# Optimization experiments

Hardware: AMD Instinct MI355X
Metric: run time of the kernel (lower is better)

## Reference

```python
import jax, jax.numpy as jnp
import numpy as np

Z_SIZE, X_SIZE = 12, 32
B, NUM_HEADS, DIM = 16, 8, 256
N = Z_SIZE * Z_SIZE + X_SIZE * X_SIZE  # 1168


def _gen_rel_index(z, x):
    # 2D concatenated (template+search) relative position index, as in the torch helper
    zh, zw = np.meshgrid(np.arange(z), np.arange(z), indexing='ij')
    xh, xw = np.meshgrid(np.arange(x), np.arange(x), indexing='ij')
    h = np.concatenate([zh.ravel(), xh.ravel()])
    w = np.concatenate([zw.ravel(), xw.ravel()])
    dh = h[:, None] - h[None, :]
    dw = w[:, None] - w[None, :]
    a = np.concatenate([np.zeros(z * z, np.int64), np.ones(x * x, np.int64)])
    n = a.shape[0]
    b = np.broadcast_to(a[:, None], (n, n))
    c = np.broadcast_to(a[None, :], (n, n))
    diff = np.stack([dh, dw, b, c], axis=-1).reshape(-1, 4)
    _, inv = np.unique(diff, axis=0, return_inverse=True)
    return inv.reshape(n, n).astype(np.int32)


def setup_inputs() -> dict:
    key = jax.random.key(0)
    k0, k1, k2, k3, k4, k5 = jax.random.split(key, 6)
    x = jax.random.normal(k0, (B, N, DIM), jnp.float32)
    mask = jax.random.randint(k1, (B, N), 0, 2) > 0  # True = masked-out key
    w_qkv = jax.random.normal(k2, (3 * DIM, DIM), jnp.float32) * 0.02
    w_proj = jax.random.normal(k3, (DIM, DIM), jnp.float32) * 0.02
    b_proj = jax.random.normal(k4, (DIM,), jnp.float32) * 0.02
    rel_index = jnp.asarray(_gen_rel_index(Z_SIZE, X_SIZE))
    num_rel = int(rel_index.max()) + 1
    rpb_table = jax.random.normal(k5, (NUM_HEADS, num_rel), jnp.float32) * 0.02
    return {"x": x, "mask": mask, "w_qkv": w_qkv, "w_proj": w_proj,
            "b_proj": b_proj, "rpb_table": rpb_table, "rel_index": rel_index}


def reference(x, mask, w_qkv, w_proj, b_proj, rpb_table, rel_index):
    Bb, Nn, C = x.shape
    H = rpb_table.shape[0]
    Dh = C // H
    scale = Dh ** -0.5
    qkv = (x @ w_qkv.T).reshape(Bb, Nn, 3, H, Dh)
    qkv = jnp.transpose(qkv, (2, 0, 3, 1, 4))  # [3, B, H, N, Dh]
    q, k, v = qkv[0], qkv[1], qkv[2]
    attn = jnp.einsum('bhnd,bhmd->bhnm', q, k) * scale
    attn = attn + rpb_table[:, rel_index][None]           # gathered rel-pos bias [1,H,N,N]
    attn = jnp.where(mask[:, None, None, :], -jnp.inf, attn)
    attn = jax.nn.softmax(attn, axis=-1)
    out = jnp.einsum('bhnm,bhmd->bnhd', attn, v).reshape(Bb, Nn, C)
    return out @ w_proj.T + b_proj
```

## Files before the change

kernel.cpp:

```cpp
#include <hip/hip_runtime.h>
#include <hip/hip_bf16.h>

#define BATCH 16
#define NH 8
#define NSEQ 1168
#define NPAD 1184
#define DH 32
#define DMODEL 256
#define MTOK (BATCH*NSEQ)
#define LOG2E 1.4426950408889634f
#define QSCALE_L2 (0.17677669529663687f * 1.4426950408889634f)
#define NRELCAP 8448

typedef __bf16 bf16_t;
typedef __bf16 bf16x8 __attribute__((ext_vector_type(8)));
typedef __bf16 bf16x4 __attribute__((ext_vector_type(4)));
typedef __bf16 bf16x2 __attribute__((ext_vector_type(2)));
typedef float  f32x4  __attribute__((ext_vector_type(4)));

__device__ __forceinline__ f32x4 mfma16(bf16x8 a, bf16x8 b, f32x4 c) {
    return __builtin_amdgcn_mfma_f32_16x16x32_bf16(a, b, c, 0, 0, 0);
}

__device__ __forceinline__ float fexp2(float x) {
#if __has_builtin(__builtin_amdgcn_exp2f)
    return __builtin_amdgcn_exp2f(x);
#else
    return exp2f(x);
#endif
}

__global__ __launch_bounds__(256) void mask_probe(const unsigned char* __restrict__ m,
                                                  int* __restrict__ flag) {
    int nbytes = BATCH * NSEQ;
    int stride = gridDim.x * blockDim.x;
    int acc = 0;
    for (int i = blockIdx.x * blockDim.x + threadIdx.x; i < nbytes; i += stride)
        if ((i & 3) && m[i]) acc = 1;
    if (__any(acc)) {
        if ((threadIdx.x & 63) == 0) atomicOr(flag, 1);
    }
}

__global__ __launch_bounds__(256) void mask_expand(const void* __restrict__ mraw,
                                                   const int* __restrict__ flag,
                                                   unsigned short* __restrict__ mask16) {
    int t = blockIdx.x * blockDim.x + threadIdx.x;
    if (t >= BATCH * NPAD) return;
    int b = t / NPAD, k = t - b * NPAD;
    bool masked = true;
    if (k < NSEQ) {
        if (*flag) masked = ((const unsigned char*)mraw)[b * NSEQ + k] != 0;
        else       masked = ((const int*)mraw)[b * NSEQ + k] != 0;
    }
    mask16[t] = masked ? 0u : 0xFFFFu;
}

__global__ __launch_bounds__(256) void bias_build(
    const int* __restrict__ rel, const float* __restrict__ rpb,
    bf16_t* __restrict__ bias, int num_rel) {
    __shared__ float rpb_s[NRELCAP];
    int h = blockIdx.y;
    const float* rph = rpb + (size_t)h * num_rel;
    int nr = num_rel > NRELCAP ? NRELCAP : num_rel;
    for (int i = threadIdx.x; i < nr; i += 256) rpb_s[i] = rph[i] * LOG2E;
    __syncthreads();
    int q0 = blockIdx.x * 32;
    int qend = q0 + 32 > NSEQ ? NSEQ : q0 + 32;
    for (int q = q0; q < qend; ++q) {
        bf16_t* brow = bias + ((size_t)h * NSEQ + q) * NPAD;
        const int* rrow = rel + (size_t)q * NSEQ;
        for (int k4 = threadIdx.x * 4; k4 < NPAD; k4 += 1024) {
            bf16x4 w;
            if (k4 + 3 < NSEQ) {
                int4 r4 = *(const int4*)&rrow[k4];
                w[0] = (bf16_t)rpb_s[r4.x]; w[1] = (bf16_t)rpb_s[r4.y];
                w[2] = (bf16_t)rpb_s[r4.z]; w[3] = (bf16_t)rpb_s[r4.w];
            } else {
                #pragma unroll
                for (int j = 0; j < 4; ++j) {
                    int k = k4 + j;
                    w[j] = (bf16_t)((k < NSEQ) ? rpb_s[rrow[k]] : -1e30f);
                }
            }
            *(bf16x4*)&brow[k4] = w;
        }
    }
}

__global__ __launch_bounds__(256) void convert_kernel(
    const float* __restrict__ x, const float* __restrict__ wq, const float* __restrict__ wp,
    bf16_t* __restrict__ xb, bf16_t* __restrict__ wqb, bf16_t* __restrict__ wpb) {
    const int NX4 = MTOK*DMODEL/4, NQ4 = 768*256/4, NP4 = 256*256/4;
    int stride = gridDim.x * blockDim.x;
    int tid = blockIdx.x * blockDim.x + threadIdx.x;
    for (int i = tid; i < NX4; i += stride) {
        float4 f = ((const float4*)x)[i];
        bf16x4 o = { (bf16_t)f.x, (bf16_t)f.y, (bf16_t)f.z, (bf16_t)f.w };
        ((bf16x4*)xb)[i] = o;
    }
    for (int i = tid; i < NQ4; i += stride) {
        float4 f = ((const float4*)wq)[i];
        bf16x4 o = { (bf16_t)f.x, (bf16_t)f.y, (bf16_t)f.z, (bf16_t)f.w };
        ((bf16x4*)wqb)[i] = o;
    }
    for (int i = tid; i < NP4; i += stride) {
        float4 f = ((const float4*)wp)[i];
        bf16x4 o = { (bf16_t)f.x, (bf16_t)f.y, (bf16_t)f.z, (bf16_t)f.w };
        ((bf16x4*)wpb)[i] = o;
    }
}

#define GEMM_CORE(Aptr, Bptr) \
    __shared__ bf16_t As[128*32]; \
    __shared__ bf16_t Bs[128*32]; \
    int t = threadIdx.x; \
    int rowA0 = blockIdx.x * 128, rowB0 = blockIdx.y * 128; \
    int lane = t & 63, w = t >> 6; \
    int wr = (w >> 1) * 64, wc = (w & 1) * 64; \
    int lr = lane & 15, lg = lane >> 4; \
    int srow = t >> 2, scol = (t & 3) * 8; \
    f32x4 acc[4][4]; \
    { f32x4 zz = {0.f,0.f,0.f,0.f}; \
      _Pragma("unroll") for (int m = 0; m < 4; ++m) \
      _Pragma("unroll") for (int n = 0; n < 4; ++n) acc[m][n] = zz; } \
    for (int k0 = 0; k0 < 256; k0 += 32) { \
        bf16x8 ra0 = *(const bf16x8*)&Aptr[(size_t)(rowA0 + srow) * 256 + k0 + scol]; \
        bf16x8 ra1 = *(const bf16x8*)&Aptr[(size_t)(rowA0 + 64 + srow) * 256 + k0 + scol]; \
        bf16x8 rb0 = *(const bf16x8*)&Bptr[(size_t)(rowB0 + srow) * 256 + k0 + scol]; \
        bf16x8 rb1 = *(const bf16x8*)&Bptr[(size_t)(rowB0 + 64 + srow) * 256 + k0 + scol]; \
        __syncthreads(); \
        *(bf16x8*)&As[srow * 32 + scol] = ra0; \
        *(bf16x8*)&As[(64 + srow) * 32 + scol] = ra1; \
        *(bf16x8*)&Bs[srow * 32 + scol] = rb0; \
        *(bf16x8*)&Bs[(64 + srow) * 32 + scol] = rb1; \
        __syncthreads(); \
        bf16x8 af[4], bfr[4]; \
        _Pragma("unroll") for (int m = 0; m < 4; ++m) \
            af[m] = *(const bf16x8*)&As[(wr + m * 16 + lr) * 32 + lg * 8]; \
        _Pragma("unroll") for (int n = 0; n < 4; ++n) \
            bfr[n] = *(const bf16x8*)&Bs[(wc + n * 16 + lr) * 32 + lg * 8]; \
        _Pragma("unroll") for (int m = 0; m < 4; ++m) \
        _Pragma("unroll") for (int n = 0; n < 4; ++n) \
            acc[m][n] = mfma16(af[m], bfr[n], acc[m][n]); \
    }

__global__ __launch_bounds__(256) void gemm_qkv(
    const bf16_t* __restrict__ A, const bf16_t* __restrict__ Bw,
    bf16_t* __restrict__ qb, bf16_t* __restrict__ kb, bf16_t* __restrict__ vt) {
    __shared__ bf16_t TT[128][130];
    GEMM_CORE(A, Bw)
    if (rowB0 < 512) {
        #pragma unroll
        for (int m = 0; m < 4; ++m) {
            #pragma unroll
            for (int i = 0; i < 4; ++i) {
                int grow = rowA0 + wr + m * 16 + lg * 4 + i;
                int b = grow / NSEQ, nt = grow - b * NSEQ;
                #pragma unroll
                for (int n = 0; n < 4; ++n) {
                    int col = rowB0 + wc + n * 16 + lr;
                    int hh = (col >> 5) & 7, d = col & 31;
                    float v = acc[m][n][i];
                    size_t hoff = (size_t)(b * NH + hh);
                    if (col < 256) qb[(hoff * NPAD + nt) * DH + d] = (bf16_t)(v * QSCALE_L2);
                    else           kb[(hoff * NPAD + nt) * DH + d] = (bf16_t)v;
                }
            }
        }
    } else {
        #pragma unroll
        for (int m = 0; m < 4; ++m)
            #pragma unroll
            for (int i = 0; i < 4; ++i)
                #pragma unroll
                for (int n = 0; n < 4; ++n)
                    TT[wr + m * 16 + lg * 4 + i][wc + n * 16 + lr] = (bf16_t)acc[m][n][i];
        __syncthreads();
        int grow0 = rowA0 + 2 * lane;
        int b = grow0 / NSEQ, nt = grow0 - b * NSEQ;
        for (int cc = 0; cc < 32; ++cc) {
            int col = rowB0 + w * 32 + cc;
            int hh = (col >> 5) & 7, d = col & 31;
            bf16x2 v = { TT[2 * lane][w * 32 + cc], TT[2 * lane + 1][w * 32 + cc] };
            *(bf16x2*)&vt[((size_t)(b * NH + hh) * DH + d) * NPAD + nt] = v;
        }
    }
}

__global__ __launch_bounds__(256) void gemm_proj(
    const bf16_t* __restrict__ A, const bf16_t* __restrict__ Bw,
    const float* __restrict__ bias, float* __restrict__ out) {
    GEMM_CORE(A, Bw)
    #pragma unroll
    for (int m = 0; m < 4; ++m) {
        #pragma unroll
        for (int i = 0; i < 4; ++i) {
            int grow = rowA0 + wr + m * 16 + lg * 4 + i;
            #pragma unroll
            for (int n = 0; n < 4; ++n) {
                int col = rowB0 + wc + n * 16 + lr;
                out[(size_t)grow * DMODEL + col] = acc[m][n][i] + bias[col];
            }
        }
    }
}

__global__ __launch_bounds__(128) void attn_kernel(
    const bf16_t* __restrict__ qb, const bf16_t* __restrict__ kb, const bf16_t* __restrict__ vt,
    const bf16_t* __restrict__ bias, const unsigned short* __restrict__ mask16,
    bf16_t* __restrict__ att) {
    __shared__ __align__(16) bf16_t P[2][2][16][40];
    int t = threadIdx.x;
    int h = blockIdx.y, b = blockIdx.z;
    int lane = t & 63, wid = t >> 6;
    int qbase = blockIdx.x * 32 + wid * 16;
    if (qbase >= NSEQ) return;
    int lr = lane & 15, lg = lane >> 4;

    const bf16_t* qh = qb + (size_t)(b * NH + h) * NPAD * DH;
    const bf16_t* kh = kb + (size_t)(b * NH + h) * NPAD * DH;
    const bf16_t* vh = vt + (size_t)(b * NH + h) * DH * NPAD;
    const bf16_t* bh = bias + ((size_t)h * NSEQ + qbase + lr) * NPAD;
    const unsigned short* mh = mask16 + b * NPAD;

    bf16x8 qf = *(const bf16x8*)&qh[(qbase + lr) * DH + lg * 8];
    bf16x8 ones;
    #pragma unroll
    for (int j = 0; j < 8; ++j) ones[j] = (bf16_t)1.f;
    f32x4 o0 = {0.f,0.f,0.f,0.f}, o1 = {0.f,0.f,0.f,0.f}, lacc = {0.f,0.f,0.f,0.f};

    #pragma unroll 2
    for (int kt = 0; kt < NPAD / 32; ++kt) {
        int kbase = kt * 32;
        int buf = kt & 1;
        bf16x8 kf0 = *(const bf16x8*)&kh[(kbase + lr) * DH + lg * 8];
        bf16x8 kf1 = *(const bf16x8*)&kh[(kbase + 16 + lr) * DH + lg * 8];
        bf16x4 bv0 = *(const bf16x4*)&bh[kbase + 4 * lg];
        bf16x4 bv1 = *(const bf16x4*)&bh[kbase + 16 + 4 * lg];
        uint2 ma0 = *(const uint2*)&mh[kbase + 4 * lg];
        uint2 ma1 = *(const uint2*)&mh[kbase + 16 + 4 * lg];
        bf16x8 vf0 = *(const bf16x8*)&vh[(size_t)lr * NPAD + kbase + lg * 8];
        bf16x8 vf1 = *(const bf16x8*)&vh[(size_t)(16 + lr) * NPAD + kbase + lg * 8];
        f32x4 z = {0.f,0.f,0.f,0.f};
        __builtin_amdgcn_s_setprio(1);
        f32x4 s0 = mfma16(kf0, qf, z);
        f32x4 s1 = mfma16(kf1, qf, z);
        __builtin_amdgcn_s_setprio(0);
        union { bf16x4 h; uint2 u; } c0, c1;
        #pragma unroll
        for (int i = 0; i < 4; ++i) c0.h[i] = (bf16_t)fexp2(s0[i] + (float)bv0[i]);
        #pragma unroll
        for (int i = 0; i < 4; ++i) c1.h[i] = (bf16_t)fexp2(s1[i] + (float)bv1[i]);
        c0.u.x &= ma0.x; c0.u.y &= ma0.y;
        c1.u.x &= ma1.x; c1.u.y &= ma1.y;
        *(bf16x4*)&P[buf][wid][lr][4 * lg] = c0.h;
        *(bf16x4*)&P[buf][wid][lr][16 + 4 * lg] = c1.h;
        bf16x8 pf = *(const bf16x8*)&P[buf][wid][lr][lg * 8];
        __builtin_amdgcn_s_setprio(1);
        o0 = mfma16(pf, vf0, o0);
        o1 = mfma16(pf, vf1, o1);
        lacc = mfma16(pf, ones, lacc);
        __builtin_amdgcn_s_setprio(0);
    }
    #pragma unroll
    for (int i = 0; i < 4; ++i) {
        float li = 1.f / lacc[i];
        int qi = qbase + 4 * lg + i;
        size_t base = ((size_t)b * NSEQ + qi) * DMODEL + h * DH;
        att[base + lr] = (bf16_t)(o0[i] * li);
        att[base + 16 + lr] = (bf16_t)(o1[i] * li);
    }
}

extern "C" void kernel_launch(void* const* d_in, const int* in_sizes, int n_in,
                              void* d_out, int out_size, void* d_ws, size_t ws_size,
                              hipStream_t stream) {
    const float* x      = (const float*)d_in[0];
    const void*  mask   = d_in[1];
    const float* w_qkv  = (const float*)d_in[2];
    const float* w_proj = (const float*)d_in[3];
    const float* b_proj = (const float*)d_in[4];
    const float* rpb    = (const float*)d_in[5];
    const int*   rel    = (const int*)d_in[6];
    float* out = (float*)d_out;
    int num_rel = in_sizes[5] / NH;

    char* ws = (char*)d_ws;
    bf16_t* xb   = (bf16_t*)(ws + 0);
    bf16_t* wqb  = (bf16_t*)(ws + 9568256);
    bf16_t* wpb  = (bf16_t*)(ws + 9961472);
    bf16_t* qb   = (bf16_t*)(ws + 10092544);
    bf16_t* kb   = (bf16_t*)(ws + 19791872);
    bf16_t* vt   = (bf16_t*)(ws + 29491200);
    bf16_t* att  = (bf16_t*)(ws + 39190528);
    unsigned short* mask16 = (unsigned short*)(ws + 48758784);
    int*    flag = (int*)(ws + 48796672);
    bf16_t* bias = (bf16_t*)(ws + 48796736);

    hipMemsetAsync(flag, 0, 4, stream);
    mask_probe<<<dim3(32), dim3(256), 0, stream>>>((const unsigned char*)mask, flag);
    mask_expand<<<dim3((BATCH * NPAD + 255) / 256), dim3(256), 0, stream>>>(mask, flag, mask16);
    bias_build<<<dim3((NSEQ + 31) / 32, NH), dim3(256), 0, stream>>>(rel, rpb, bias, num_rel);
    convert_kernel<<<dim3(2048), dim3(256), 0, stream>>>(x, w_qkv, w_proj, xb, wqb, wpb);
    gemm_qkv<<<dim3(146, 6), dim3(256), 0, stream>>>(xb, wqb, qb, kb, vt);
    attn_kernel<<<dim3(37, NH, BATCH), dim3(128), 0, stream>>>(qb, kb, vt, bias, mask16, att);
    gemm_proj<<<dim3(146, 2), dim3(256), 0, stream>>>(att, wpb, b_proj, out);
}
```

Before: 293.1 us.

## Prefetch next attention tile, permute bias/mask layout, merge mask kernels, reorder grid

Lays out the bias and mask arrays in a per-tile permuted order so each lane can fetch its bias and mask values with one 16-byte load instead of two 8-byte loads. The attention loop now software-pipelines the K, V, bias and mask loads one tile ahead behind a sched_barrier, to hide global load latency behind the MFMA and exp work. Mask probing and expansion are merged into one per-batch kernel, which drops a memset and a launch. The attention grid is flattened with heads innermost so that blocks sharing bias rows and K/V data run closer together in time. In exchange the loop holds more registers, and the bias build now does scalar gathers.

```diff
diff --git a/kernel.cpp b/kernel.cpp
--- a/kernel.cpp
+++ b/kernel.cpp
@@ -30,30 +30,28 @@
 #endif
 }
 
-__global__ __launch_bounds__(256) void mask_probe(const unsigned char* __restrict__ m,
-                                                  int* __restrict__ flag) {
-    int nbytes = BATCH * NSEQ;
-    int stride = gridDim.x * blockDim.x;
+__global__ __launch_bounds__(256) void mask_expand(const void* __restrict__ mraw,
+                                                   unsigned short* __restrict__ mperm) {
+    __shared__ int wf[4];
+    int b = blockIdx.x, t = threadIdx.x;
+    const unsigned int* w32 = (const unsigned int*)mraw;
     int acc = 0;
-    for (int i = blockIdx.x * blockDim.x + threadIdx.x; i < nbytes; i += stride)
-        if ((i & 3) && m[i]) acc = 1;
-    if (__any(acc)) {
-        if ((threadIdx.x & 63) == 0) atomicOr(flag, 1);
-    }
-}
-
-__global__ __launch_bounds__(256) void mask_expand(const void* __restrict__ mraw,
-                                                   const int* __restrict__ flag,
-                                                   unsigned short* __restrict__ mask16) {
-    int t = blockIdx.x * blockDim.x + threadIdx.x;
-    if (t >= BATCH * NPAD) return;
-    int b = t / NPAD, k = t - b * NPAD;
-    bool masked = true;
-    if (k < NSEQ) {
-        if (*flag) masked = ((const unsigned char*)mraw)[b * NSEQ + k] != 0;
-        else       masked = ((const int*)mraw)[b * NSEQ + k] != 0;
-    }
-    mask16[t] = masked ? 0u : 0xFFFFu;
+    for (int i = t; i < (BATCH * NSEQ) / 4; i += 256)
+        if (w32[i] & 0xFFFFFF00u) acc = 1;
+    int any = __any(acc) ? 1 : 0;
+    if ((t & 63) == 0) wf[t >> 6] = any;
+    __syncthreads();
+    int u8mode = wf[0] | wf[1] | wf[2] | wf[3];
+    for (int idx = t; idx < NPAD; idx += 256) {
+        int kt = idx >> 5, r = idx & 31, g = r >> 3, jj = r & 7;
+        int k = kt * 32 + (jj < 4 ? 4 * g + jj : 16 + 4 * g + (jj - 4));
+        bool masked = true;
+        if (k < NSEQ) {
+            if (u8mode) masked = ((const unsigned char*)mraw)[b * NSEQ + k] != 0;
+            else        masked = ((const int*)mraw)[b * NSEQ + k] != 0;
+        }
+        mperm[b * NPAD + idx] = masked ? 0u : 0xFFFFu;
+    }
 }
 
 __global__ __launch_bounds__(256) void bias_build(
@@ -70,20 +68,15 @@
     for (int q = q0; q < qend; ++q) {
         bf16_t* brow = bias + ((size_t)h * NSEQ + q) * NPAD;
         const int* rrow = rel + (size_t)q * NSEQ;
-        for (int k4 = threadIdx.x * 4; k4 < NPAD; k4 += 1024) {
-            bf16x4 w;
-            if (k4 + 3 < NSEQ) {
-                int4 r4 = *(const int4*)&rrow[k4];
-                w[0] = (bf16_t)rpb_s[r4.x]; w[1] = (bf16_t)rpb_s[r4.y];
-                w[2] = (bf16_t)rpb_s[r4.z]; w[3] = (bf16_t)rpb_s[r4.w];
-            } else {
-                #pragma unroll
-                for (int j = 0; j < 4; ++j) {
-                    int k = k4 + j;
-                    w[j] = (bf16_t)((k < NSEQ) ? rpb_s[rrow[k]] : -1e30f);
-                }
+        for (int idx = threadIdx.x; idx < NPAD / 8; idx += 256) {
+            int kt = idx >> 2, g = idx & 3;
+            bf16x8 w;
+            #pragma unroll
+            for (int jj = 0; jj < 8; ++jj) {
+                int k = kt * 32 + (jj < 4 ? 4 * g + jj : 16 + 4 * g + (jj - 4));
+                w[jj] = (bf16_t)((k < NSEQ) ? rpb_s[rrow[k]] : -1e30f);
             }
-            *(bf16x4*)&brow[k4] = w;
+            *(bf16x8*)&brow[idx * 8] = w;
         }
     }
 }
@@ -208,13 +201,16 @@
 
 __global__ __launch_bounds__(128) void attn_kernel(
     const bf16_t* __restrict__ qb, const bf16_t* __restrict__ kb, const bf16_t* __restrict__ vt,
-    const bf16_t* __restrict__ bias, const unsigned short* __restrict__ mask16,
+    const bf16_t* __restrict__ bias, const unsigned short* __restrict__ mperm,
     bf16_t* __restrict__ att) {
     __shared__ __align__(16) bf16_t P[2][2][16][40];
     int t = threadIdx.x;
-    int h = blockIdx.y, b = blockIdx.z;
+    int L = blockIdx.x;
+    int h = L & 7;
+    int j = L >> 3;
+    int b = j / 37, qt = j - b * 37;
     int lane = t & 63, wid = t >> 6;
-    int qbase = blockIdx.x * 32 + wid * 16;
+    int qbase = qt * 32 + wid * 16;
     if (qbase >= NSEQ) return;
     int lr = lane & 15, lg = lane >> 4;
 
@@ -222,46 +218,55 @@
     const bf16_t* kh = kb + (size_t)(b * NH + h) * NPAD * DH;
     const bf16_t* vh = vt + (size_t)(b * NH + h) * DH * NPAD;
     const bf16_t* bh = bias + ((size_t)h * NSEQ + qbase + lr) * NPAD;
-    const unsigned short* mh = mask16 + b * NPAD;
+    const unsigned short* mh = mperm + b * NPAD;
 
     bf16x8 qf = *(const bf16x8*)&qh[(qbase + lr) * DH + lg * 8];
     bf16x8 ones;
     #pragma unroll
-    for (int j = 0; j < 8; ++j) ones[j] = (bf16_t)1.f;
+    for (int jj = 0; jj < 8; ++jj) ones[jj] = (bf16_t)1.f;
     f32x4 o0 = {0.f,0.f,0.f,0.f}, o1 = {0.f,0.f,0.f,0.f}, lacc = {0.f,0.f,0.f,0.f};
 
+    const int NT = NPAD / 32;
+    bf16x8 kf0 = *(const bf16x8*)&kh[lr * DH + lg * 8];
+    bf16x8 kf1 = *(const bf16x8*)&kh[(16 + lr) * DH + lg * 8];
+    bf16x8 bv  = *(const bf16x8*)&bh[8 * lg];
+    uint4  mm  = *(const uint4*)&mh[8 * lg];
+    bf16x8 vf0 = *(const bf16x8*)&vh[(size_t)lr * NPAD + lg * 8];
+    bf16x8 vf1 = *(const bf16x8*)&vh[(size_t)(16 + lr) * NPAD + lg * 8];
+
     #pragma unroll 2
-    for (int kt = 0; kt < NPAD / 32; ++kt) {
+    for (int kt = 0; kt < NT; ++kt) {
         int kbase = kt * 32;
+        int nb = (kt + 1 < NT ? kt + 1 : kt) * 32;
+        bf16x8 nkf0 = *(const bf16x8*)&kh[(nb + lr) * DH + lg * 8];
+        bf16x8 nkf1 = *(const bf16x8*)&kh[(nb + 16 + lr) * DH + lg * 8];
+        bf16x8 nbv  = *(const bf16x8*)&bh[nb + 8 * lg];
+        uint4  nmm  = *(const uint4*)&mh[nb + 8 * lg];
+        bf16x8 nvf0 = *(const bf16x8*)&vh[(size_t)lr * NPAD + nb + lg * 8];
+        bf16x8 nvf1 = *(const bf16x8*)&vh[(size_t)(16 + lr) * NPAD + nb + lg * 8];
+        __builtin_amdgcn_sched_barrier(0);
         int buf = kt & 1;
-        bf16x8 kf0 = *(const bf16x8*)&kh[(kbase + lr) * DH + lg * 8];
-        bf16x8 kf1 = *(const bf16x8*)&kh[(kbase + 16 + lr) * DH + lg * 8];
-        bf16x4 bv0 = *(const bf16x4*)&bh[kbase + 4 * lg];
-        bf16x4 bv1 = *(const bf16x4*)&bh[kbase + 16 + 4 * lg];
-        uint2 ma0 = *(const uint2*)&mh[kbase + 4 * lg];
-        uint2 ma1 = *(const uint2*)&mh[kbase + 16 + 4 * lg];
-        bf16x8 vf0 = *(const bf16x8*)&vh[(size_t)lr * NPAD + kbase + lg * 8];
-        bf16x8 vf1 = *(const bf16x8*)&vh[(size_t)(16 + lr) * NPAD + kbase + lg * 8];
         f32x4 z = {0.f,0.f,0.f,0.f};
         __builtin_amdgcn_s_setprio(1);
         f32x4 s0 = mfma16(kf0, qf, z);
         f32x4 s1 = mfma16(kf1, qf, z);
         __builtin_amdgcn_s_setprio(0);
-        union { bf16x4 h; uint2 u; } c0, c1;
-        #pragma unroll
-        for (int i = 0; i < 4; ++i) c0.h[i] = (bf16_t)fexp2(s0[i] + (float)bv0[i]);
-        #pragma unroll
-        for (int i = 0; i < 4; ++i) c1.h[i] = (bf16_t)fexp2(s1[i] + (float)bv1[i]);
-        c0.u.x &= ma0.x; c0.u.y &= ma0.y;
-        c1.u.x &= ma1.x; c1.u.y &= ma1.y;
-        *(bf16x4*)&P[buf][wid][lr][4 * lg] = c0.h;
-        *(bf16x4*)&P[buf][wid][lr][16 + 4 * lg] = c1.h;
+        union { bf16x4 hh; uint2 u; } c0, c1;
+        #pragma unroll
+        for (int i = 0; i < 4; ++i) c0.hh[i] = (bf16_t)fexp2(s0[i] + (float)bv[i]);
+        #pragma unroll
+        for (int i = 0; i < 4; ++i) c1.hh[i] = (bf16_t)fexp2(s1[i] + (float)bv[4 + i]);
+        c0.u.x &= mm.x; c0.u.y &= mm.y;
+        c1.u.x &= mm.z; c1.u.y &= mm.w;
+        *(bf16x4*)&P[buf][wid][lr][4 * lg] = c0.hh;
+        *(bf16x4*)&P[buf][wid][lr][16 + 4 * lg] = c1.hh;
         bf16x8 pf = *(const bf16x8*)&P[buf][wid][lr][lg * 8];
         __builtin_amdgcn_s_setprio(1);
         o0 = mfma16(pf, vf0, o0);
         o1 = mfma16(pf, vf1, o1);
         lacc = mfma16(pf, ones, lacc);
         __builtin_amdgcn_s_setprio(0);
+        kf0 = nkf0; kf1 = nkf1; bv = nbv; mm = nmm; vf0 = nvf0; vf1 = nvf1;
     }
     #pragma unroll
     for (int i = 0; i < 4; ++i) {
@@ -294,16 +299,13 @@
     bf16_t* kb   = (bf16_t*)(ws + 19791872);
     bf16_t* vt   = (bf16_t*)(ws + 29491200);
     bf16_t* att  = (bf16_t*)(ws + 39190528);
-    unsigned short* mask16 = (unsigned short*)(ws + 48758784);
-    int*    flag = (int*)(ws + 48796672);
-    bf16_t* bias = (bf16_t*)(ws + 48796736);
-
-    hipMemsetAsync(flag, 0, 4, stream);
-    mask_probe<<<dim3(32), dim3(256), 0, stream>>>((const unsigned char*)mask, flag);
-    mask_expand<<<dim3((BATCH * NPAD + 255) / 256), dim3(256), 0, stream>>>(mask, flag, mask16);
+    unsigned short* mperm = (unsigned short*)(ws + 48758784);
+    bf16_t* bias = (bf16_t*)(ws + 48796672);
+
+    mask_expand<<<dim3(BATCH), dim3(256), 0, stream>>>(mask, mperm);
     bias_build<<<dim3((NSEQ + 31) / 32, NH), dim3(256), 0, stream>>>(rel, rpb, bias, num_rel);
     convert_kernel<<<dim3(2048), dim3(256), 0, stream>>>(x, w_qkv, w_proj, xb, wqb, wpb);
     gemm_qkv<<<dim3(146, 6), dim3(256), 0, stream>>>(xb, wqb, qb, kb, vt);
-    attn_kernel<<<dim3(37, NH, BATCH), dim3(128), 0, stream>>>(qb, kb, vt, bias, mask16, att);
+    attn_kernel<<<dim3(8 * 16 * 37), dim3(128), 0, stream>>>(qb, kb, vt, bias, mperm, att);
     gemm_proj<<<dim3(146, 2), dim3(256), 0, stream>>>(att, wpb, b_proj, out);
 }
```

After: 282.1 us. 3.8% less time.
